# Kernel optimization log

Measured on AMD Instinct MI355X. Metric: run time of the kernel, lower is better.

The kernel has to match this reference:

```python
import jax, jax.numpy as jnp
from jax import lax
import numpy as np

OBS_DIM, PROJ, HID, LAT = 128, 64, 256, 24
B, T = 1024, 256


def setup_inputs() -> dict:
    key = jax.random.key(0)
    ks = jax.random.split(key, 10)
    obs = jax.random.normal(ks[0], (B, T, OBS_DIM), dtype=jnp.float32)
    is_init = jax.random.randint(ks[1], (B, T, 1), 0, 2) > 0
    hx = jnp.zeros((B, HID), dtype=jnp.float32)
    # params (fan-in scaled)
    W_in = jax.random.normal(ks[2], (OBS_DIM, PROJ), dtype=jnp.float32) / np.sqrt(OBS_DIM)
    b_in = jnp.zeros((PROJ,), dtype=jnp.float32)
    W_ih = jax.random.normal(ks[3], (PROJ, 3 * HID), dtype=jnp.float32) / np.sqrt(PROJ)
    b_ih = jnp.zeros((3 * HID,), dtype=jnp.float32)
    W_hh = jax.random.normal(ks[4], (HID, 3 * HID), dtype=jnp.float32) / np.sqrt(HID)
    b_hh = jnp.zeros((3 * HID,), dtype=jnp.float32)
    W_out = jax.random.normal(ks[5], (HID, LAT), dtype=jnp.float32) / np.sqrt(HID)
    b_out = jnp.zeros((LAT,), dtype=jnp.float32)
    return dict(obs=obs, is_init=is_init, hx=hx, W_in=W_in, b_in=b_in,
                W_ih=W_ih, b_ih=b_ih, W_hh=W_hh, b_hh=b_hh,
                W_out=W_out, b_out=b_out)


def reference(obs, is_init, hx, W_in, b_in, W_ih, b_ih, W_hh, b_hh, W_out, b_out):
    # input projection: [B,T,OBS] -> [B,T,64]
    x = obs @ W_in + b_in
    # precompute input-side gates once: [B,T,3H]
    gx = jnp.swapaxes(x @ W_ih + b_ih, 0, 1)           # [T,B,3H]
    mask = jnp.swapaxes(is_init.astype(hx.dtype), 0, 1)  # [T,B,1]

    def step(h, inp):
        g, m = inp
        h = h * (1.0 - m)                # episode-reset masking
        gh = h @ W_hh + b_hh             # [B,3H]
        gxr, gxz, gxn = jnp.split(g, 3, axis=-1)
        ghr, ghz, ghn = jnp.split(gh, 3, axis=-1)
        r = jax.nn.sigmoid(gxr + ghr)
        z = jax.nn.sigmoid(gxz + ghz)
        n = jnp.tanh(gxn + r * ghn)
        h_new = (1.0 - z) * n + z * h
        return h_new, h_new

    h_final, ys = lax.scan(step, hx, (gx, mask))
    seq = jnp.swapaxes(ys, 0, 1)         # [B,T,H]
    mish = seq * jnp.tanh(jax.nn.softplus(seq))
    out = mish @ W_out + b_out           # [B,T,LAT]
    return out, h_final
```

## Files before the change

### kernel.cpp

```cpp
#include <hip/hip_runtime.h>
#include <cstdint>
#include <cstddef>

#define OBS_DIMM 128
#define PROJJ    64
#define HIDD     256
#define LATT     24
#define BBATCH   1024
#define TTIME    256
#define NGATE    768
#define MBLK     16
#define CHUNK    64
#define NGROUP   64
#define NCHUNK   4
#define HSTR     264

using bf16x8 = __attribute__((ext_vector_type(8))) short;
using bf16x4 = __attribute__((ext_vector_type(4))) short;
using f32x4  = __attribute__((ext_vector_type(4))) float;

static __device__ __forceinline__ unsigned short f2bf(float f) {
    unsigned u = __builtin_bit_cast(unsigned, f);
    u += 0x7fffu + ((u >> 16) & 1u);
    return (unsigned short)(u >> 16);
}
static __device__ __forceinline__ float bf2f(unsigned short h) {
    return __builtin_bit_cast(float, ((unsigned)h) << 16);
}
static __device__ __forceinline__ float fexp2(float x) { return __builtin_amdgcn_exp2f(x); }
static __device__ __forceinline__ float frcp (float x) { return __builtin_amdgcn_rcpf(x); }
static __device__ __forceinline__ float sigmoid_(float x) { return frcp(1.f + fexp2(-1.44269504f * x)); }
static __device__ __forceinline__ float tanh_(float x)    { return 1.f - 2.f * frcp(fexp2(2.88539008f * x) + 1.f); }
static __device__ __forceinline__ unsigned short mish_bf(float x) {
    float ex = fexp2(1.44269504f * x);
    float t1 = 1.f + ex;
    return f2bf(x * (1.f - 2.f * frcp(t1 * t1 + 1.f)));
}

static __device__ __forceinline__ void bar_lgkm() {
    asm volatile("s_waitcnt lgkmcnt(0)\n\ts_barrier" ::: "memory");
}

#define MFMA16(a, b, c) __builtin_amdgcn_mfma_f32_16x16x32_bf16((a), (b), (c), 0, 0, 0)

__global__ void prep_kernel(const float* __restrict__ W_in, const float* __restrict__ b_in,
                            const float* __restrict__ W_ih, const float* __restrict__ b_ih,
                            const float* __restrict__ W_hh, const float* __restrict__ W_out,
                            unsigned short* __restrict__ wsWhh, unsigned short* __restrict__ wsWih,
                            unsigned short* __restrict__ wsWin, unsigned short* __restrict__ wsWo,
                            float* __restrict__ wsBx) {
    int idx = blockIdx.x * 256 + threadIdx.x;
    if (idx < 196608) {
        int f = idx >> 9, rem = idx & 511, l = rem >> 3, jj = rem & 7;
        int q = l >> 4, c16 = l & 15;
        int g = f % 3, f2 = f / 3, i = f2 & 1, f3 = f2 >> 1;
        int kt = f3 & 7, w = f3 >> 3;
        int s5 = q * 8 + jj;
        int k = kt * 32 + ((s5 & 1) << 4) + (s5 >> 1);
        int n = g * 256 + (2 * w + i) * 16 + c16;
        wsWhh[idx] = f2bf(W_hh[k * NGATE + n]);
    } else if (idx < 245760) {
        int d = idx - 196608;
        int f = d >> 9, rem = d & 511, l = rem >> 3, jj = rem & 7;
        int q = l >> 4, c16 = l & 15;
        int g = f % 3, f2 = f / 3, i = f2 & 1, f3 = f2 >> 1;
        int kt = f3 & 1, w = f3 >> 1;
        int k = kt * 32 + q * 8 + jj;
        int n = g * 256 + (2 * w + i) * 16 + c16;
        wsWih[d] = f2bf(W_ih[k * NGATE + n]);
    } else if (idx < 253952) {
        int d = idx - 245760;
        int f = d >> 9, rem = d & 511, l = rem >> 3, jj = rem & 7;
        int q = l >> 4, nl = l & 15;
        int nt = f & 3, kt = f >> 2;
        int k = kt * 32 + q * 8 + jj;
        int n = nt * 16 + nl;
        wsWin[d] = f2bf(W_in[k * PROJJ + n]);
    } else if (idx < 262144) {
        int d = idx - 253952;
        int f = d >> 9, rem = d & 511, l = rem >> 3, jj = rem & 7;
        int q = l >> 4, nl = l & 15;
        int kt = f & 7, nt = f >> 3;
        int s5 = q * 8 + jj;
        int k = kt * 32 + ((s5 & 1) << 4) + (s5 >> 1);
        int n = nt * 16 + nl;
        wsWo[d] = f2bf((n < LATT) ? W_out[k * LATT + n] : 0.f);
    } else if (idx < 262912) {
        int n = idx - 262144;
        float s = b_ih[n];
        for (int j = 0; j < PROJJ; ++j) s += b_in[j] * W_ih[j * NGATE + n];
        wsBx[n] = s;
    }
}

__global__ __launch_bounds__(256)
void xproj_kernel(const float* __restrict__ obs, const unsigned short* __restrict__ wsWin,
                  unsigned short* __restrict__ xf) {
    __shared__ __align__(16) unsigned short sXP[4][1040];
    const int tid = threadIdx.x, w = tid >> 6, lane = tid & 63, q = lane >> 4, c16 = lane & 15;
    const int tile = blockIdx.x * 4 + w;
    const int g = tile >> 8, t = tile & 255;
    const float* op = obs + ((size_t)(g * 16 + c16) * TTIME + t) * OBS_DIMM + q * 8;
    bf16x8 a[4];
#pragma unroll
    for (int kt = 0; kt < 4; ++kt) {
        float4 u0 = *(const float4*)(op + kt * 32);
        float4 u1 = *(const float4*)(op + kt * 32 + 4);
        bf16x8 v;
        v[0] = (short)f2bf(u0.x); v[1] = (short)f2bf(u0.y);
        v[2] = (short)f2bf(u0.z); v[3] = (short)f2bf(u0.w);
        v[4] = (short)f2bf(u1.x); v[5] = (short)f2bf(u1.y);
        v[6] = (short)f2bf(u1.z); v[7] = (short)f2bf(u1.w);
        a[kt] = v;
    }
    f32x4 acc[4];
#pragma unroll
    for (int nt = 0; nt < 4; ++nt) acc[nt] = (f32x4){0.f, 0.f, 0.f, 0.f};
#pragma unroll
    for (int kt = 0; kt < 4; ++kt)
#pragma unroll
        for (int nt = 0; nt < 4; ++nt)
            acc[nt] = MFMA16(a[kt], *(const bf16x8*)(wsWin + (kt * 4 + nt) * 512 + lane * 8), acc[nt]);
#pragma unroll
    for (int nt = 0; nt < 4; ++nt) {
        int unit = nt * 16 + c16;
        int ktp = unit >> 5, qp = (unit >> 3) & 3, jjp = unit & 7;
#pragma unroll
        for (int r = 0; r < 4; ++r)
            sXP[w][(qp * 16 + q * 4 + r) * 16 + ktp * 8 + jjp] = f2bf(acc[nt][r]);
    }
    __syncthreads();
    unsigned short* dst = xf + (size_t)tile * 1024 + lane * 16;
    *(bf16x8*)dst       = *(const bf16x8*)(sXP[w] + lane * 16);
    *(bf16x8*)(dst + 8) = *(const bf16x8*)(sXP[w] + lane * 16 + 8);
}

__global__ __launch_bounds__(512, 2)
void gru_kernel(const int* __restrict__ is_init, const float* __restrict__ hx,
                const float* __restrict__ b_hh, const float* __restrict__ b_out,
                const unsigned short* __restrict__ wsWhh, const unsigned short* __restrict__ wsWih,
                const unsigned short* __restrict__ wsWo, const float* __restrict__ wsBx,
                const unsigned short* __restrict__ xf,
                float* __restrict__ out, float* __restrict__ hfin) {
    __shared__ __align__(16) unsigned short sWih[49152];
    __shared__ __align__(16) unsigned short sWo[8192];
    __shared__ __align__(16) unsigned short sH[2][MBLK * HSTR];
    __shared__ __align__(16) unsigned short sM[3][MBLK * HSTR];
    __shared__ __align__(16) float sBias[1056];
    __shared__ unsigned sInit[MBLK][8];
    __shared__ int sT;

    const int tid  = threadIdx.x;
    const int w    = tid >> 6;
    const int lane = tid & 63;
    const int q    = lane >> 4;
    const int c16  = lane & 15;
    const int bid  = blockIdx.x;
    const int g    = bid & (NGROUP - 1);
    const int ch   = bid >> 6;
    const int b0   = g * MBLK;
    const int t0   = ch * CHUNK;
    const int tend = t0 + CHUNK;

    const unsigned short* whh_p = wsWhh + (size_t)w * 24576 + lane * 8;
    bf16x8 Whh[48];
#pragma unroll
    for (int f = 0; f < 48; ++f)
        Whh[f] = *(const bf16x8*)(whh_p + (size_t)f * 512);

    {
        const uint4* s1 = (const uint4*)wsWih; uint4* d1 = (uint4*)sWih;
#pragma unroll
        for (int r = 0; r < 12; ++r) d1[r * 512 + tid] = s1[r * 512 + tid];
        const uint4* s3 = (const uint4*)wsWo;  uint4* d3 = (uint4*)sWo;
#pragma unroll
        for (int r = 0; r < 2; ++r) d3[r * 512 + tid] = s3[r * 512 + tid];
    }
    if (tid < 256) {
        sBias[tid]       = wsBx[tid] + b_hh[tid];
        sBias[256 + tid] = wsBx[HIDD + tid] + b_hh[HIDD + tid];
        sBias[512 + tid] = wsBx[2 * HIDD + tid];
        sBias[768 + tid] = b_hh[2 * HIDD + tid];
    } else if (tid < 288) {
        int col = tid - 256;
        sBias[1024 + col] = (col < LATT) ? b_out[col] : 0.f;
    }
    if (tid < 128) {
        int b = tid >> 3, wd = tid & 7;
        unsigned m = 0;
        const int* ip = is_init + (size_t)(b0 + b) * TTIME + wd * 32;
#pragma unroll
        for (int j = 0; j < 32; ++j) m |= (ip[j] != 0 ? 1u : 0u) << j;
        sInit[b][wd] = m;
    }
    if (tid == 0) sT = (ch == 0) ? 0 : 0x7fffffff;
    __syncthreads();

    if (ch > 0 && tid < MBLK) {
        int fs = 0;
        for (int wi = (t0 >> 5) - 1; wi >= 0; --wi) {
            unsigned m = sInit[tid][wi];
            if (wi == 0) m &= ~1u;
            if (m) { fs = wi * 32 + 31 - __builtin_clz(m); break; }
        }
        atomicMin(&sT, fs);
    }
    __syncthreads();
    const int tstart = sT;

    unsigned hReg[4];
#pragma unroll
    for (int r = 0; r < 4; ++r) {
        int b = q * 4 + r;
        unsigned rbit = (sInit[b][tstart >> 5] >> (tstart & 31)) & 1u;
        float h0v = 0.f, h1v = 0.f;
        if (tstart == 0 && !rbit) {
            const float* hp = hx + (size_t)(b0 + b) * HIDD;
            h0v = hp[2 * w * 16 + c16];
            h1v = hp[(2 * w + 1) * 16 + c16];
        }
        unsigned pk = (unsigned)f2bf(h0v) | ((unsigned)f2bf(h1v) << 16);
        hReg[r] = pk;
        ((unsigned*)sH[0])[b * 132 + w * 16 + c16] = pk;
    }
    bf16x8 X0, X1;
    {
        const unsigned short* xp = xf + (size_t)(g * 256 + tstart) * 1024 + lane * 16;
        X0 = *(const bf16x8*)xp; X1 = *(const bf16x8*)(xp + 8);
    }
    const unsigned short* wihp = sWih + w * 6144 + lane * 8;
    unsigned short* sHr = sH[0];
    unsigned short* sHw = sH[1];
    unsigned short* pWm = sM[tstart % 3];
    unsigned short* pR1 = sM[(tstart + 2) % 3];
    unsigned short* pR2 = sM[(tstart + 1) % 3];
    __syncthreads();

    f32x4 accR[2], accZ[2], accXN[2], accHN[2];
    auto accfill = [&]() {
#pragma unroll
        for (int i = 0; i < 2; ++i) {
            int u = (2 * w + i) * 16 + c16;
            float vR = sBias[u], vZ = sBias[256 + u], vX = sBias[512 + u], vH = sBias[768 + u];
            accR[i]  = (f32x4){vR, vR, vR, vR};
            accZ[i]  = (f32x4){vZ, vZ, vZ, vZ};
            accXN[i] = (f32x4){vX, vX, vX, vX};
            accHN[i] = (f32x4){vH, vH, vH, vH};
            accR[i]  = MFMA16(X0, *(const bf16x8*)(wihp + (i * 3 + 0) * 512), accR[i]);
            accZ[i]  = MFMA16(X0, *(const bf16x8*)(wihp + (i * 3 + 1) * 512), accZ[i]);
            accXN[i] = MFMA16(X0, *(const bf16x8*)(wihp + (i * 3 + 2) * 512), accXN[i]);
            accR[i]  = MFMA16(X1, *(const bf16x8*)(wihp + (6 + i * 3 + 0) * 512), accR[i]);
            accZ[i]  = MFMA16(X1, *(const bf16x8*)(wihp + (6 + i * 3 + 1) * 512), accZ[i]);
            accXN[i] = MFMA16(X1, *(const bf16x8*)(wihp + (6 + i * 3 + 2) * 512), accXN[i]);
        }
    };
    accfill();

    for (int t = tstart; t < tend; ++t) {
        {
            int tn = (t + 1 < TTIME) ? t + 1 : TTIME - 1;
            const unsigned short* xp = xf + (size_t)(g * 256 + tn) * 1024 + lane * 16;
            X0 = *(const bf16x8*)xp; X1 = *(const bf16x8*)(xp + 8);
        }
#pragma unroll
        for (int kt = 0; kt < 8; ++kt) {
            bf16x8 a = *(const bf16x8*)(sHr + c16 * HSTR + kt * 32 + q * 8);
#pragma unroll
            for (int i = 0; i < 2; ++i) {
                accR[i]  = MFMA16(a, Whh[kt * 6 + i * 3 + 0], accR[i]);
                accZ[i]  = MFMA16(a, Whh[kt * 6 + i * 3 + 1], accZ[i]);
                accHN[i] = MFMA16(a, Whh[kt * 6 + i * 3 + 2], accHN[i]);
            }
        }
        f32x4 oa;
        const bool doO = (t >= t0 + 2) && ((w >> 1) == (t & 3));
        if (doO) {
            int nt = w & 1;
            float bo = sBias[1024 + nt * 16 + c16];
            oa = (f32x4){bo, bo, bo, bo};
            const unsigned short* smp = pR2 + c16 * HSTR + q * 8;
#pragma unroll
            for (int kt = 0; kt < 8; ++kt)
                oa = MFMA16(*(const bf16x8*)(smp + kt * 32),
                            *(const bf16x8*)(sWo + (nt * 8 + kt) * 512 + lane * 8), oa);
        }
        int m4 = 0;
        if (t + 1 < tend) {
            int wd = (t + 1) >> 5, bt = (t + 1) & 31;
#pragma unroll
            for (int r = 0; r < 4; ++r)
                m4 |= (int)((sInit[q * 4 + r][wd] >> bt) & 1u) << r;
        }
        const bool emit = (t >= t0);
#pragma unroll
        for (int r = 0; r < 4; ++r) {
            int bl = q * 4 + r;
            float hs0 = bf2f((unsigned short)(hReg[r] & 0xffffu));
            float hs1 = bf2f((unsigned short)(hReg[r] >> 16));
            float rr0 = sigmoid_(accR[0][r]), rr1 = sigmoid_(accR[1][r]);
            float zz0 = sigmoid_(accZ[0][r]), zz1 = sigmoid_(accZ[1][r]);
            float nn0 = tanh_(accXN[0][r] + rr0 * accHN[0][r]);
            float nn1 = tanh_(accXN[1][r] + rr1 * accHN[1][r]);
            float h0 = (1.f - zz0) * nn0 + zz0 * hs0;
            float h1 = (1.f - zz1) * nn1 + zz1 * hs1;
            if (emit)
                ((unsigned*)pWm)[bl * 132 + w * 16 + c16] =
                    (unsigned)mish_bf(h0) | ((unsigned)mish_bf(h1) << 16);
            if ((m4 >> r) & 1) { h0 = 0.f; h1 = 0.f; }
            unsigned pk = (unsigned)f2bf(h0) | ((unsigned)f2bf(h1) << 16);
            hReg[r] = pk;
            ((unsigned*)sHw)[bl * 132 + w * 16 + c16] = pk;
        }
        if (doO) {
            int nt = w & 1, col = nt * 16 + c16, tb = t - 2;
            if (col < LATT) {
#pragma unroll
                for (int r = 0; r < 4; ++r)
                    out[((size_t)(b0 + q * 4 + r) * TTIME + tb) * LATT + col] = oa[r];
            }
        }
        if (t + 1 < tend) accfill();
        bar_lgkm();
        { unsigned short* tp = sHr; sHr = sHw; sHw = tp; }
        { unsigned short* tp = pWm; pWm = pR2; pR2 = pR1; pR1 = tp; }
    }

    if (w < 4) {
        int nt = w & 1;
        unsigned short* pR = (w < 2) ? pR2 : pR1;
        int tb = (w < 2) ? tend - 2 : tend - 1;
        float bo = sBias[1024 + nt * 16 + c16];
        f32x4 oa2 = (f32x4){bo, bo, bo, bo};
        const unsigned short* smp = pR + c16 * HSTR + q * 8;
#pragma unroll
        for (int kt = 0; kt < 8; ++kt)
            oa2 = MFMA16(*(const bf16x8*)(smp + kt * 32),
                         *(const bf16x8*)(sWo + (nt * 8 + kt) * 512 + lane * 8), oa2);
        int col = nt * 16 + c16;
        if (col < LATT) {
#pragma unroll
            for (int r = 0; r < 4; ++r)
                out[((size_t)(b0 + q * 4 + r) * TTIME + tb) * LATT + col] = oa2[r];
        }
    }
    if (ch == NCHUNK - 1) {
#pragma unroll
        for (int r = 0; r < 4; ++r) {
            float* hp = hfin + (size_t)(b0 + q * 4 + r) * HIDD;
            hp[2 * w * 16 + c16]       = bf2f((unsigned short)(hReg[r] & 0xffffu));
            hp[(2 * w + 1) * 16 + c16] = bf2f((unsigned short)(hReg[r] >> 16));
        }
    }
}

extern "C" void kernel_launch(void* const* d_in, const int* in_sizes, int n_in,
                              void* d_out, int out_size, void* d_ws, size_t ws_size,
                              hipStream_t stream) {
    const float* obs    = (const float*)d_in[0];
    const int*   isini  = (const int*)d_in[1];
    const float* hx     = (const float*)d_in[2];
    const float* W_in   = (const float*)d_in[3];
    const float* b_in   = (const float*)d_in[4];
    const float* W_ih   = (const float*)d_in[5];
    const float* b_ih   = (const float*)d_in[6];
    const float* W_hh   = (const float*)d_in[7];
    const float* b_hh   = (const float*)d_in[8];
    const float* W_out  = (const float*)d_in[9];
    const float* b_out  = (const float*)d_in[10];

    unsigned short* xfbuf = (unsigned short*)d_ws;
    unsigned short* wsWhh = xfbuf + (size_t)BBATCH * TTIME * 64;
    unsigned short* wsWih = wsWhh + 196608;
    unsigned short* wsWin = wsWih + 49152;
    unsigned short* wsWo  = wsWin + 8192;
    float*          wsBx  = (float*)(wsWo + 8192);

    float* outp = (float*)d_out;
    float* hfin = outp + (size_t)BBATCH * TTIME * LATT;

    prep_kernel<<<1027, 256, 0, stream>>>(W_in, b_in, W_ih, b_ih, W_hh, W_out,
                                          wsWhh, wsWih, wsWin, wsWo, wsBx);
    xproj_kernel<<<4096, 256, 0, stream>>>(obs, wsWin, xfbuf);
    gru_kernel<<<256, 512, 0, stream>>>(isini, hx, b_hh, b_out,
                                        wsWhh, wsWih, wsWo, wsBx, xfbuf, outp, hfin);
}
```

Baseline: 491.4 us.

## Coalesce obs loads through LDS in xproj and use packed bf16 conversion

The xproj kernel now stages the W_in fragment and a 16-batch by 8-timestep slab of obs in LDS, reading obs with coalesced float4 rows instead of scattered per-lane strided loads. Each wave then runs two timestep tiles, and the grid is halved. The GRU kernel hoists its per-lane bias loads out of the per-step accfill and uses the hardware v_cvt_pk_bf16_f32 instruction instead of manual rounding for the h and mish packing. The packed conversion's rounding may differ slightly from the software round-to-nearest-even, and the xproj kernel uses more LDS.

```diff
diff --git a/kernel.cpp b/kernel.cpp
--- a/kernel.cpp
+++ b/kernel.cpp
@@ -16,7 +16,6 @@
 #define HSTR     264
 
 using bf16x8 = __attribute__((ext_vector_type(8))) short;
-using bf16x4 = __attribute__((ext_vector_type(4))) short;
 using f32x4  = __attribute__((ext_vector_type(4))) float;
 
 static __device__ __forceinline__ unsigned short f2bf(float f) {
@@ -27,14 +26,19 @@
 static __device__ __forceinline__ float bf2f(unsigned short h) {
     return __builtin_bit_cast(float, ((unsigned)h) << 16);
 }
+static __device__ __forceinline__ unsigned cvt_pk_bf16(float lo, float hi) {
+    unsigned r;
+    asm("v_cvt_pk_bf16_f32 %0, %1, %2" : "=v"(r) : "v"(lo), "v"(hi));
+    return r;
+}
 static __device__ __forceinline__ float fexp2(float x) { return __builtin_amdgcn_exp2f(x); }
 static __device__ __forceinline__ float frcp (float x) { return __builtin_amdgcn_rcpf(x); }
 static __device__ __forceinline__ float sigmoid_(float x) { return frcp(1.f + fexp2(-1.44269504f * x)); }
 static __device__ __forceinline__ float tanh_(float x)    { return 1.f - 2.f * frcp(fexp2(2.88539008f * x) + 1.f); }
-static __device__ __forceinline__ unsigned short mish_bf(float x) {
+static __device__ __forceinline__ float mish_f(float x) {
     float ex = fexp2(1.44269504f * x);
     float t1 = 1.f + ex;
-    return f2bf(x * (1.f - 2.f * frcp(t1 * t1 + 1.f)));
+    return x * (1.f - 2.f * frcp(t1 * t1 + 1.f));
 }
 
 static __device__ __forceinline__ void bar_lgkm() {
@@ -96,43 +100,56 @@
 __global__ __launch_bounds__(256)
 void xproj_kernel(const float* __restrict__ obs, const unsigned short* __restrict__ wsWin,
                   unsigned short* __restrict__ xf) {
+    __shared__ __align__(16) unsigned short ldsO[8 * 16 * 136];
+    __shared__ __align__(16) unsigned short sWin[8192];
     __shared__ __align__(16) unsigned short sXP[4][1040];
     const int tid = threadIdx.x, w = tid >> 6, lane = tid & 63, q = lane >> 4, c16 = lane & 15;
-    const int tile = blockIdx.x * 4 + w;
-    const int g = tile >> 8, t = tile & 255;
-    const float* op = obs + ((size_t)(g * 16 + c16) * TTIME + t) * OBS_DIMM + q * 8;
-    bf16x8 a[4];
-#pragma unroll
-    for (int kt = 0; kt < 4; ++kt) {
-        float4 u0 = *(const float4*)(op + kt * 32);
-        float4 u1 = *(const float4*)(op + kt * 32 + 4);
-        bf16x8 v;
-        v[0] = (short)f2bf(u0.x); v[1] = (short)f2bf(u0.y);
-        v[2] = (short)f2bf(u0.z); v[3] = (short)f2bf(u0.w);
-        v[4] = (short)f2bf(u1.x); v[5] = (short)f2bf(u1.y);
-        v[6] = (short)f2bf(u1.z); v[7] = (short)f2bf(u1.w);
-        a[kt] = v;
-    }
-    f32x4 acc[4];
-#pragma unroll
-    for (int nt = 0; nt < 4; ++nt) acc[nt] = (f32x4){0.f, 0.f, 0.f, 0.f};
-#pragma unroll
-    for (int kt = 0; kt < 4; ++kt)
-#pragma unroll
-        for (int nt = 0; nt < 4; ++nt)
-            acc[nt] = MFMA16(a[kt], *(const bf16x8*)(wsWin + (kt * 4 + nt) * 512 + lane * 8), acc[nt]);
-#pragma unroll
-    for (int nt = 0; nt < 4; ++nt) {
-        int unit = nt * 16 + c16;
-        int ktp = unit >> 5, qp = (unit >> 3) & 3, jjp = unit & 7;
-#pragma unroll
-        for (int r = 0; r < 4; ++r)
-            sXP[w][(qp * 16 + q * 4 + r) * 16 + ktp * 8 + jjp] = f2bf(acc[nt][r]);
+    const int bid = blockIdx.x;
+    const int g = bid >> 5, tc = bid & 31;
+    const int t0x = tc * 8, b0x = g * 16;
+
+    {
+        const uint4* s = (const uint4*)wsWin; uint4* d = (uint4*)sWin;
+#pragma unroll
+        for (int r = 0; r < 4; ++r) d[r * 256 + tid] = s[r * 256 + tid];
+    }
+    {
+        const int tl = tid >> 5, f4 = tid & 31;
+        const float* base = obs + ((size_t)b0x * TTIME + t0x + tl) * OBS_DIMM + f4 * 4;
+#pragma unroll
+        for (int p = 0; p < 16; ++p) {
+            float4 v = *(const float4*)(base + (size_t)p * TTIME * OBS_DIMM);
+            unsigned lo = cvt_pk_bf16(v.x, v.y);
+            unsigned hi = cvt_pk_bf16(v.z, v.w);
+            *(uint2*)(ldsO + (tl * 16 + p) * 136 + f4 * 4) = make_uint2(lo, hi);
+        }
     }
     __syncthreads();
-    unsigned short* dst = xf + (size_t)tile * 1024 + lane * 16;
-    *(bf16x8*)dst       = *(const bf16x8*)(sXP[w] + lane * 16);
-    *(bf16x8*)(dst + 8) = *(const bf16x8*)(sXP[w] + lane * 16 + 8);
+
+    for (int s = 0; s < 2; ++s) {
+        const int tl = w * 2 + s;
+        f32x4 acc[4];
+#pragma unroll
+        for (int nt = 0; nt < 4; ++nt) acc[nt] = (f32x4){0.f, 0.f, 0.f, 0.f};
+#pragma unroll
+        for (int kt = 0; kt < 4; ++kt) {
+            bf16x8 a = *(const bf16x8*)(ldsO + (tl * 16 + c16) * 136 + kt * 32 + q * 8);
+#pragma unroll
+            for (int nt = 0; nt < 4; ++nt)
+                acc[nt] = MFMA16(a, *(const bf16x8*)(sWin + (kt * 4 + nt) * 512 + lane * 8), acc[nt]);
+        }
+#pragma unroll
+        for (int nt = 0; nt < 4; ++nt) {
+            int unit = nt * 16 + c16;
+            int ktp = unit >> 5, qp = (unit >> 3) & 3, jjp = unit & 7;
+#pragma unroll
+            for (int r = 0; r < 4; ++r)
+                sXP[w][(qp * 16 + q * 4 + r) * 16 + ktp * 8 + jjp] = f2bf(acc[nt][r]);
+        }
+        unsigned short* dst = xf + (size_t)(g * 256 + t0x + tl) * 1024 + lane * 16;
+        *(bf16x8*)dst       = *(const bf16x8*)(sXP[w] + lane * 16);
+        *(bf16x8*)(dst + 8) = *(const bf16x8*)(sXP[w] + lane * 16 + 8);
+    }
 }
 
 __global__ __launch_bounds__(512, 2)
@@ -196,6 +213,12 @@
     if (tid == 0) sT = (ch == 0) ? 0 : 0x7fffffff;
     __syncthreads();
 
+    const int u0 = 2 * w * 16 + c16, u1 = (2 * w + 1) * 16 + c16;
+    const float bR0 = sBias[u0],       bR1 = sBias[u1];
+    const float bZ0 = sBias[256 + u0], bZ1 = sBias[256 + u1];
+    const float bX0 = sBias[512 + u0], bX1 = sBias[512 + u1];
+    const float bH0 = sBias[768 + u0], bH1 = sBias[768 + u1];
+
     if (ch > 0 && tid < MBLK) {
         int fs = 0;
         for (int wi = (t0 >> 5) - 1; wi >= 0; --wi) {
@@ -238,14 +261,16 @@
 
     f32x4 accR[2], accZ[2], accXN[2], accHN[2];
     auto accfill = [&]() {
+        accR[0]  = (f32x4){bR0, bR0, bR0, bR0};
+        accZ[0]  = (f32x4){bZ0, bZ0, bZ0, bZ0};
+        accXN[0] = (f32x4){bX0, bX0, bX0, bX0};
+        accHN[0] = (f32x4){bH0, bH0, bH0, bH0};
+        accR[1]  = (f32x4){bR1, bR1, bR1, bR1};
+        accZ[1]  = (f32x4){bZ1, bZ1, bZ1, bZ1};
+        accXN[1] = (f32x4){bX1, bX1, bX1, bX1};
+        accHN[1] = (f32x4){bH1, bH1, bH1, bH1};
 #pragma unroll
         for (int i = 0; i < 2; ++i) {
-            int u = (2 * w + i) * 16 + c16;
-            float vR = sBias[u], vZ = sBias[256 + u], vX = sBias[512 + u], vH = sBias[768 + u];
-            accR[i]  = (f32x4){vR, vR, vR, vR};
-            accZ[i]  = (f32x4){vZ, vZ, vZ, vZ};
-            accXN[i] = (f32x4){vX, vX, vX, vX};
-            accHN[i] = (f32x4){vH, vH, vH, vH};
             accR[i]  = MFMA16(X0, *(const bf16x8*)(wihp + (i * 3 + 0) * 512), accR[i]);
             accZ[i]  = MFMA16(X0, *(const bf16x8*)(wihp + (i * 3 + 1) * 512), accZ[i]);
             accXN[i] = MFMA16(X0, *(const bf16x8*)(wihp + (i * 3 + 2) * 512), accXN[i]);
@@ -305,9 +330,9 @@
             float h1 = (1.f - zz1) * nn1 + zz1 * hs1;
             if (emit)
                 ((unsigned*)pWm)[bl * 132 + w * 16 + c16] =
-                    (unsigned)mish_bf(h0) | ((unsigned)mish_bf(h1) << 16);
+                    cvt_pk_bf16(mish_f(h0), mish_f(h1));
             if ((m4 >> r) & 1) { h0 = 0.f; h1 = 0.f; }
-            unsigned pk = (unsigned)f2bf(h0) | ((unsigned)f2bf(h1) << 16);
+            unsigned pk = cvt_pk_bf16(h0, h1);
             hReg[r] = pk;
             ((unsigned*)sHw)[bl * 132 + w * 16 + c16] = pk;
         }
@@ -380,7 +405,7 @@
 
     prep_kernel<<<1027, 256, 0, stream>>>(W_in, b_in, W_ih, b_ih, W_hh, W_out,
                                           wsWhh, wsWih, wsWin, wsWo, wsBx);
-    xproj_kernel<<<4096, 256, 0, stream>>>(obs, wsWin, xfbuf);
+    xproj_kernel<<<2048, 256, 0, stream>>>(obs, wsWin, xfbuf);
     gru_kernel<<<256, 512, 0, stream>>>(isini, hx, b_hh, b_out,
                                         wsWhh, wsWih, wsWo, wsBx, xfbuf, outp, hfin);
 }
```

Result: slower. 627.5 us (+27.7%).
